# Performance work log

Measured on AMD Instinct MI355X. Metric: run time of the kernel, lower is better.

## Reference

```python
import jax, jax.numpy as jnp
import numpy as np

B, S, DIM = 2, 2048, 1536
H = 12            # n_heads (SIGMA)
HD = DIM // H     # head_dim = 128
SIGMA = 12        # anchors per query: 6 local + 4 strided + 2 global
STRIDE_STEP = 5   # SOPFR


def setup_inputs() -> dict:
    key = jax.random.key(0)
    k0, k1, k2 = jax.random.split(key, 3)
    s = 0.02
    return {
        "x": jax.random.normal(k0, (B, S, DIM), dtype=jnp.float32),
        "Wqkv": jax.random.normal(k1, (DIM, 3 * DIM), dtype=jnp.float32) * s,
        "bqkv": jnp.zeros((3 * DIM,), dtype=jnp.float32),
        "Wout": jax.random.normal(k2, (DIM, DIM), dtype=jnp.float32) * s,
        "bout": jnp.zeros((DIM,), dtype=jnp.float32),
        # Egyptian-fraction init: [W_LOCAL, W_STRIDE, W_GLOBAL] = [1/2, 1/3, 1/6]
        "group_scale": jnp.array([0.5, 1.0 / 3.0, 1.0 / 6.0], dtype=jnp.float32),
    }


def _anchor_indices(seq_len):
    # (S, 12) int32: 6 local offsets, 4 strided offsets, then global {0, S-1}
    pos = jnp.arange(seq_len, dtype=jnp.int32)
    offs = jnp.array([-3, -2, -1, 1, 2, 3,
                      -2 * STRIDE_STEP, -STRIDE_STEP, STRIDE_STEP, 2 * STRIDE_STEP],
                     dtype=jnp.int32)
    a = jnp.clip(pos[:, None] + offs[None, :], 0, seq_len - 1)
    glob = jnp.stack([jnp.zeros_like(pos), jnp.full_like(pos, seq_len - 1)], axis=1)
    return jnp.concatenate([a, glob], axis=1)


def reference(x, Wqkv, bqkv, Wout, bout, group_scale):
    b, s, d_model = x.shape
    # QKV projection -> (3, B, H, S, HD)
    qkv = (x @ Wqkv + bqkv).reshape(b, s, 3, H, HD).transpose(2, 0, 3, 1, 4)
    q, k, v = qkv[0], qkv[1], qkv[2]
    scale = HD ** -0.5

    anchor = _anchor_indices(s)                 # (S, SIGMA)
    k_anchors = jnp.take(k, anchor, axis=2)     # (B, H, S, SIGMA, HD)
    v_anchors = jnp.take(v, anchor, axis=2)     # (B, H, S, SIGMA, HD)

    attn = jnp.einsum('bhsd,bhsad->bhsa', q, k_anchors) * scale

    gw = jax.nn.softmax(group_scale)            # (3,)
    weight_per_anchor = jnp.concatenate([
        jnp.broadcast_to(gw[0], (6,)),   # local
        jnp.broadcast_to(gw[1], (4,)),   # strided
        jnp.broadcast_to(gw[2], (2,)),   # global
    ])                                          # (SIGMA,)
    attn = attn + jnp.log(weight_per_anchor)    # broadcast over (B,H,S,·)

    attn = jax.nn.softmax(attn, axis=-1)
    attn = jnp.nan_to_num(attn, nan=0.0)

    out = jnp.einsum('bhsa,bhsad->bhsd', attn, v_anchors)
    out = out.transpose(0, 2, 1, 3).reshape(b, s, d_model)
    return out @ Wout + bout
```

## Files before the change

kernel.cpp:

```cpp
#include <hip/hip_runtime.h>
#include <hip/hip_bf16.h>
#include <cstdint>
#include <math.h>

#define B_    2
#define S_    2048
#define DIM_  1536
#define H_    12
#define HD_   128
#define TRI_  4608
#define M_    4096

typedef __attribute__((ext_vector_type(8))) __bf16 bf16x8;
typedef __attribute__((ext_vector_type(4))) __bf16 bf16x4;
typedef __attribute__((ext_vector_type(4))) float  floatx4;

typedef __attribute__((address_space(3))) uint8_t       lds_u8;
typedef const __attribute__((address_space(1))) uint8_t glob_u8;

__global__ __launch_bounds__(256) void prep(const float* __restrict__ W1,
                                            __bf16* __restrict__ O1,
                                            const float* __restrict__ W2,
                                            __bf16* __restrict__ O2,
                                            const float* __restrict__ x,
                                            __bf16* __restrict__ x_bf,
                                            float* __restrict__ outz) {
    const int T1 = (TRI_ / 64) * (DIM_ / 64);
    const int T2 = (DIM_ / 64) * (DIM_ / 64);
    const int NC = (M_ * DIM_) / 1024;
    int blk = blockIdx.x;
    const int t = threadIdx.x;

    if (blk >= T1 + T2) {
        blk -= T1 + T2;
        if (blk < NC) {
            int i = blk * 256 + t;
            float4 v = ((const float4*)x)[i];
            bf16x4 o;
            o.x = (__bf16)v.x; o.y = (__bf16)v.y; o.z = (__bf16)v.z; o.w = (__bf16)v.w;
            *(bf16x4*)(x_bf + (size_t)i * 4) = o;
        } else {
            blk -= NC;
            int i = blk * 256 + t;
            ((float4*)outz)[i] = make_float4(0.f, 0.f, 0.f, 0.f);
        }
        return;
    }

    const float* in; __bf16* out; int R, C, c0, r0;
    if (blk < T1) {
        in = W1; out = O1; R = DIM_; C = TRI_;
        c0 = (blk % (TRI_ / 64)) * 64; r0 = (blk / (TRI_ / 64)) * 64;
    } else {
        blk -= T1;
        in = W2; out = O2; R = DIM_; C = DIM_;
        c0 = (blk % (DIM_ / 64)) * 64; r0 = (blk / (DIM_ / 64)) * 64;
    }
    __shared__ float tile[64][65];
    const int c4 = t & 15, r = t >> 4;
    #pragma unroll
    for (int i = 0; i < 64; i += 16) {
        float4 v = *(const float4*)&in[(size_t)(r0 + r + i) * C + c0 + c4 * 4];
        tile[r + i][c4 * 4 + 0] = v.x;
        tile[r + i][c4 * 4 + 1] = v.y;
        tile[r + i][c4 * 4 + 2] = v.z;
        tile[r + i][c4 * 4 + 3] = v.w;
    }
    __syncthreads();
    const int cc = t >> 2, ch = t & 3;
    #pragma unroll
    for (int cho = 0; cho < 8; cho += 4) {
        int chh = ch + cho;
        bf16x8 o;
        #pragma unroll
        for (int k = 0; k < 8; ++k) o[k] = (__bf16)tile[chh * 8 + k][cc];
        *(bf16x8*)&out[(size_t)(c0 + cc) * R + r0 + chh * 8] = o;
    }
}

__global__ __launch_bounds__(256, 3) void gemm_qkv(const __bf16* __restrict__ A,
                                                   const __bf16* __restrict__ Bt,
                                                   const float*  __restrict__ bias,
                                                   __bf16* __restrict__ Cout,
                                                   int Mdim, int Ndim, int Kdim) {
    __shared__ __align__(16) __bf16 sA[128 * 64];
    __shared__ __align__(16) __bf16 sB[192 * 64];

    const int ntiles = Ndim / 192;
    const int tile_n = blockIdx.x % ntiles;
    const int tile_m = blockIdx.x / ntiles;
    const int m0 = tile_m << 7, n0 = tile_n * 192;

    const int tid  = threadIdx.x;
    const int lane = tid & 63;
    const int wave = tid >> 6;
    const int wm = (wave >> 1) * 64;
    const int wn = (wave & 1) * 96;

    floatx4 acc[4][6] = {};

    const int lr8 = lane >> 3;
    const int swz = (((lane & 7) ^ lr8) * 8);
    const int row  = lane & 15;
    const int quad = lane >> 4;
    const int xr   = row & 7;

    for (int k0 = 0; k0 < Kdim; k0 += 64) {
        #pragma unroll
        for (int c = 0; c < 4; ++c) {
            int r0 = wave * 32 + c * 8;
            const __bf16* ga = A + (size_t)(m0 + r0 + lr8) * Kdim + k0 + swz;
            __builtin_amdgcn_global_load_lds((glob_u8*)ga, (lds_u8*)&sA[r0 * 64], 16, 0, 0);
        }
        #pragma unroll
        for (int c = 0; c < 6; ++c) {
            int r0 = wave * 48 + c * 8;
            const __bf16* gb = Bt + (size_t)(n0 + r0 + lr8) * Kdim + k0 + swz;
            __builtin_amdgcn_global_load_lds((glob_u8*)gb, (lds_u8*)&sB[r0 * 64], 16, 0, 0);
        }
        __syncthreads();

        #pragma unroll
        for (int ks = 0; ks < 2; ++ks) {
            const int ko = ((ks * 4 + quad) ^ xr) * 8;
            bf16x8 af[4], bfr[6];
            #pragma unroll
            for (int i = 0; i < 4; ++i)
                af[i] = *(const bf16x8*)&sA[(wm + i * 16 + row) * 64 + ko];
            #pragma unroll
            for (int j = 0; j < 6; ++j)
                bfr[j] = *(const bf16x8*)&sB[(wn + j * 16 + row) * 64 + ko];
            #pragma unroll
            for (int i = 0; i < 4; ++i)
                #pragma unroll
                for (int j = 0; j < 6; ++j)
                    acc[i][j] = __builtin_amdgcn_mfma_f32_16x16x32_bf16(af[i], bfr[j], acc[i][j], 0, 0, 0);
        }
        __syncthreads();
    }

    #pragma unroll
    for (int j = 0; j < 6; ++j) {
        int gc = n0 + wn + j * 16 + row;
        float bv = bias[gc];
        #pragma unroll
        for (int i = 0; i < 4; ++i) {
            #pragma unroll
            for (int r = 0; r < 4; ++r) {
                int gr = m0 + wm + i * 16 + quad * 4 + r;
                Cout[(size_t)gr * Ndim + gc] = (__bf16)(acc[i][j][r] + bv);
            }
        }
    }
}

__global__ __launch_bounds__(256, 3) void gemm_out(const __bf16* __restrict__ A,
                                                   const __bf16* __restrict__ Bt,
                                                   const float*  __restrict__ bias,
                                                   float* __restrict__ Cout,
                                                   int Mdim, int Ndim, int Kdim) {
    __shared__ __align__(16) __bf16 sA[128 * 64];
    __shared__ __align__(16) __bf16 sB[128 * 64];

    const int ntiles = Ndim >> 7;
    const int half = (Mdim >> 7) * ntiles;
    int idx = blockIdx.x;
    const int slice = idx >= half;
    if (slice) idx -= half;
    const int tile_n = idx % ntiles;
    const int tile_m = idx / ntiles;
    const int m0 = tile_m << 7, n0 = tile_n << 7;
    const int kbeg = slice ? (Kdim >> 1) : 0;
    const int kend = kbeg + (Kdim >> 1);

    const int tid  = threadIdx.x;
    const int lane = tid & 63;
    const int wave = tid >> 6;
    const int wm = (wave >> 1) * 64;
    const int wn = (wave & 1) * 64;

    floatx4 acc[4][4] = {};

    const int lr8 = lane >> 3;
    const int swz = (((lane & 7) ^ lr8) * 8);
    const int row  = lane & 15;
    const int quad = lane >> 4;
    const int xr   = row & 7;

    for (int k0 = kbeg; k0 < kend; k0 += 64) {
        #pragma unroll
        for (int c = 0; c < 4; ++c) {
            int r0 = wave * 32 + c * 8;
            const __bf16* ga = A + (size_t)(m0 + r0 + lr8) * Kdim + k0 + swz;
            __builtin_amdgcn_global_load_lds((glob_u8*)ga, (lds_u8*)&sA[r0 * 64], 16, 0, 0);
            const __bf16* gb = Bt + (size_t)(n0 + r0 + lr8) * Kdim + k0 + swz;
            __builtin_amdgcn_global_load_lds((glob_u8*)gb, (lds_u8*)&sB[r0 * 64], 16, 0, 0);
        }
        __syncthreads();

        #pragma unroll
        for (int ks = 0; ks < 2; ++ks) {
            const int ko = ((ks * 4 + quad) ^ xr) * 8;
            bf16x8 af[4], bfr[4];
            #pragma unroll
            for (int i = 0; i < 4; ++i) {
                af[i]  = *(const bf16x8*)&sA[(wm + i * 16 + row) * 64 + ko];
                bfr[i] = *(const bf16x8*)&sB[(wn + i * 16 + row) * 64 + ko];
            }
            #pragma unroll
            for (int i = 0; i < 4; ++i)
                #pragma unroll
                for (int j = 0; j < 4; ++j)
                    acc[i][j] = __builtin_amdgcn_mfma_f32_16x16x32_bf16(af[i], bfr[j], acc[i][j], 0, 0, 0);
        }
        __syncthreads();
    }

    #pragma unroll
    for (int j = 0; j < 4; ++j) {
        int gc = n0 + wn + j * 16 + row;
        float bv = slice ? 0.f : bias[gc];
        #pragma unroll
        for (int i = 0; i < 4; ++i) {
            #pragma unroll
            for (int r = 0; r < 4; ++r) {
                int gr = m0 + wm + i * 16 + quad * 4 + r;
                atomicAdd(&Cout[(size_t)gr * Ndim + gc], acc[i][j][r] + bv);
            }
        }
    }
}

__global__ __launch_bounds__(192) void anchor_attn(const __bf16* __restrict__ qkv,
                                                   const float* __restrict__ group_scale,
                                                   __bf16* __restrict__ attn_out) {
    const int bs = blockIdx.x;
    const int b  = bs >> 11;
    const int s  = bs & 2047;
    const int t  = threadIdx.x;
    const int h  = t >> 4;
    const int tt = t & 15;
    const int d0 = tt * 8;

    float g0 = group_scale[0], g1 = group_scale[1], g2 = group_scale[2];
    float gm = fmaxf(g0, fmaxf(g1, g2));
    float e0 = __expf(g0 - gm), e1 = __expf(g1 - gm), e2 = __expf(g2 - gm);
    float ls = __logf(e0 + e1 + e2);
    float lw0 = g0 - gm - ls, lw1 = g1 - gm - ls, lw2 = g2 - gm - ls;

    const size_t rowbase = (size_t)(b * S_ + s) * TRI_ + h * HD_ + d0;
    bf16x8 qv = *(const bf16x8*)(qkv + rowbase);
    float q[8];
    #pragma unroll
    for (int k = 0; k < 8; ++k) q[k] = (float)qv[k];

    int idxs[12];
    const int offs[10] = {-3, -2, -1, 1, 2, 3, -10, -5, 5, 10};
    #pragma unroll
    for (int a = 0; a < 10; ++a) {
        int tgt = s + offs[a];
        idxs[a] = min(max(tgt, 0), S_ - 1);
    }
    idxs[10] = 0; idxs[11] = S_ - 1;

    const float scale = 0.08838834764831845f;
    float p[12];
    float mx = -1e30f;
    #pragma unroll
    for (int a = 0; a < 12; ++a) {
        const __bf16* kp = qkv + (size_t)(b * S_ + idxs[a]) * TRI_ + DIM_ + h * HD_ + d0;
        bf16x8 kv = *(const bf16x8*)kp;
        float d = 0.f;
        #pragma unroll
        for (int k = 0; k < 8; ++k) d += q[k] * (float)kv[k];
        d += __shfl_xor(d, 1); d += __shfl_xor(d, 2);
        d += __shfl_xor(d, 4); d += __shfl_xor(d, 8);
        float sc = d * scale + (a < 6 ? lw0 : (a < 10 ? lw1 : lw2));
        p[a] = sc;
        mx = fmaxf(mx, sc);
    }
    float l = 0.f;
    #pragma unroll
    for (int a = 0; a < 12; ++a) { p[a] = __expf(p[a] - mx); l += p[a]; }
    float inv = 1.0f / l;

    float o[8] = {};
    #pragma unroll
    for (int a = 0; a < 12; ++a) {
        const __bf16* vp = qkv + (size_t)(b * S_ + idxs[a]) * TRI_ + 2 * DIM_ + h * HD_ + d0;
        bf16x8 vv = *(const bf16x8*)vp;
        #pragma unroll
        for (int k = 0; k < 8; ++k) o[k] += p[a] * (float)vv[k];
    }
    bf16x8 ov;
    #pragma unroll
    for (int k = 0; k < 8; ++k) ov[k] = (__bf16)(o[k] * inv);
    *(bf16x8*)(attn_out + (size_t)(b * S_ + s) * DIM_ + h * HD_ + d0) = ov;
}

extern "C" void kernel_launch(void* const* d_in, const int* in_sizes, int n_in,
                              void* d_out, int out_size, void* d_ws, size_t ws_size,
                              hipStream_t stream) {
    const float* x    = (const float*)d_in[0];
    const float* Wqkv = (const float*)d_in[1];
    const float* bqkv = (const float*)d_in[2];
    const float* Wout = (const float*)d_in[3];
    const float* bout = (const float*)d_in[4];
    const float* gsc  = (const float*)d_in[5];
    float* out = (float*)d_out;

    char* ws = (char*)d_ws;
    __bf16* x_bf   = (__bf16*)(ws);
    __bf16* WqkvT  = (__bf16*)(ws + 12582912);
    __bf16* WoutT  = (__bf16*)(ws + 12582912 + 14155776);
    __bf16* qkv    = (__bf16*)(ws + 12582912 + 14155776 + 4718592);
    __bf16* attn   = (__bf16*)(ws + 12582912 + 14155776 + 4718592 + 37748736);

    {
        int nblk = (TRI_ / 64) * (DIM_ / 64) + (DIM_ / 64) * (DIM_ / 64)
                 + (M_ * DIM_) / 1024 + (M_ * DIM_) / 1024;
        prep<<<nblk, 256, 0, stream>>>(Wqkv, WqkvT, Wout, WoutT, x, x_bf, out);
    }

    gemm_qkv<<<(M_ / 128) * (TRI_ / 192), 256, 0, stream>>>(
        x_bf, WqkvT, bqkv, qkv, M_, TRI_, DIM_);

    anchor_attn<<<B_ * S_, 192, 0, stream>>>(qkv, gsc, attn);

    gemm_out<<<2 * (M_ / 128) * (DIM_ / 128), 256, 0, stream>>>(
        attn, WoutT, bout, out, M_, DIM_, DIM_);
}
```

Baseline: 252.7 us.

## Drop split-K atomics in output GEMM and use 128-wide K tiles

The output projection no longer splits K across two block slices that accumulated with float atomics. Each block now computes its full 128x128 tile over all of K and writes results with plain stores. Because the output no longer needs a zero-initialised buffer, the zeroing pass in the prep kernel is removed. The K tile per stage doubles to 128, with a matching LDS swizzle, so there are half as many barrier-separated iterations. The trade-off is half as many blocks (384 tiles) for the 256-CU part, 64KB of LDS per block, and the dropped occupancy hint of 3 blocks per CU.

New measurement: 230.1 us. 8.9% less time.

```diff
diff --git a/kernel.cpp b/kernel.cpp
--- a/kernel.cpp
+++ b/kernel.cpp
@@ -23,27 +23,19 @@
                                             const float* __restrict__ W2,
                                             __bf16* __restrict__ O2,
                                             const float* __restrict__ x,
-                                            __bf16* __restrict__ x_bf,
-                                            float* __restrict__ outz) {
+                                            __bf16* __restrict__ x_bf) {
     const int T1 = (TRI_ / 64) * (DIM_ / 64);
     const int T2 = (DIM_ / 64) * (DIM_ / 64);
-    const int NC = (M_ * DIM_) / 1024;
     int blk = blockIdx.x;
     const int t = threadIdx.x;
 
     if (blk >= T1 + T2) {
         blk -= T1 + T2;
-        if (blk < NC) {
-            int i = blk * 256 + t;
-            float4 v = ((const float4*)x)[i];
-            bf16x4 o;
-            o.x = (__bf16)v.x; o.y = (__bf16)v.y; o.z = (__bf16)v.z; o.w = (__bf16)v.w;
-            *(bf16x4*)(x_bf + (size_t)i * 4) = o;
-        } else {
-            blk -= NC;
-            int i = blk * 256 + t;
-            ((float4*)outz)[i] = make_float4(0.f, 0.f, 0.f, 0.f);
-        }
+        int i = blk * 256 + t;
+        float4 v = ((const float4*)x)[i];
+        bf16x4 o;
+        o.x = (__bf16)v.x; o.y = (__bf16)v.y; o.z = (__bf16)v.z; o.w = (__bf16)v.w;
+        *(bf16x4*)(x_bf + (size_t)i * 4) = o;
         return;
     }
 
@@ -154,24 +146,18 @@
     }
 }
 
-__global__ __launch_bounds__(256, 3) void gemm_out(const __bf16* __restrict__ A,
-                                                   const __bf16* __restrict__ Bt,
-                                                   const float*  __restrict__ bias,
-                                                   float* __restrict__ Cout,
-                                                   int Mdim, int Ndim, int Kdim) {
-    __shared__ __align__(16) __bf16 sA[128 * 64];
-    __shared__ __align__(16) __bf16 sB[128 * 64];
+__global__ __launch_bounds__(256) void gemm_out(const __bf16* __restrict__ A,
+                                                const __bf16* __restrict__ Bt,
+                                                const float*  __restrict__ bias,
+                                                float* __restrict__ Cout,
+                                                int Mdim, int Ndim, int Kdim) {
+    __shared__ __align__(16) __bf16 sA[128 * 128];
+    __shared__ __align__(16) __bf16 sB[128 * 128];
 
     const int ntiles = Ndim >> 7;
-    const int half = (Mdim >> 7) * ntiles;
-    int idx = blockIdx.x;
-    const int slice = idx >= half;
-    if (slice) idx -= half;
-    const int tile_n = idx % ntiles;
-    const int tile_m = idx / ntiles;
+    const int tile_n = blockIdx.x % ntiles;
+    const int tile_m = blockIdx.x / ntiles;
     const int m0 = tile_m << 7, n0 = tile_n << 7;
-    const int kbeg = slice ? (Kdim >> 1) : 0;
-    const int kend = kbeg + (Kdim >> 1);
 
     const int tid  = threadIdx.x;
     const int lane = tid & 63;
@@ -181,31 +167,34 @@
 
     floatx4 acc[4][4] = {};
 
-    const int lr8 = lane >> 3;
-    const int swz = (((lane & 7) ^ lr8) * 8);
+    const int lr4 = lane >> 4;
+    const int lc  = lane & 15;
+    int swz[4];
+    #pragma unroll
+    for (int v = 0; v < 4; ++v) swz[v] = (lc ^ (v * 4 + lr4)) * 8;
+
     const int row  = lane & 15;
     const int quad = lane >> 4;
-    const int xr   = row & 7;
-
-    for (int k0 = kbeg; k0 < kend; k0 += 64) {
-        #pragma unroll
-        for (int c = 0; c < 4; ++c) {
-            int r0 = wave * 32 + c * 8;
-            const __bf16* ga = A + (size_t)(m0 + r0 + lr8) * Kdim + k0 + swz;
-            __builtin_amdgcn_global_load_lds((glob_u8*)ga, (lds_u8*)&sA[r0 * 64], 16, 0, 0);
-            const __bf16* gb = Bt + (size_t)(n0 + r0 + lr8) * Kdim + k0 + swz;
-            __builtin_amdgcn_global_load_lds((glob_u8*)gb, (lds_u8*)&sB[r0 * 64], 16, 0, 0);
+
+    for (int k0 = 0; k0 < Kdim; k0 += 128) {
+        #pragma unroll
+        for (int c = 0; c < 8; ++c) {
+            int r0 = wave * 32 + c * 4;
+            const __bf16* ga = A + (size_t)(m0 + r0 + lr4) * Kdim + k0 + swz[c & 3];
+            __builtin_amdgcn_global_load_lds((glob_u8*)ga, (lds_u8*)&sA[r0 * 128], 16, 0, 0);
+            const __bf16* gb = Bt + (size_t)(n0 + r0 + lr4) * Kdim + k0 + swz[c & 3];
+            __builtin_amdgcn_global_load_lds((glob_u8*)gb, (lds_u8*)&sB[r0 * 128], 16, 0, 0);
         }
         __syncthreads();
 
         #pragma unroll
-        for (int ks = 0; ks < 2; ++ks) {
-            const int ko = ((ks * 4 + quad) ^ xr) * 8;
+        for (int ks = 0; ks < 4; ++ks) {
+            const int ck = ((ks * 4 + quad) ^ row) * 8;
             bf16x8 af[4], bfr[4];
             #pragma unroll
             for (int i = 0; i < 4; ++i) {
-                af[i]  = *(const bf16x8*)&sA[(wm + i * 16 + row) * 64 + ko];
-                bfr[i] = *(const bf16x8*)&sB[(wn + i * 16 + row) * 64 + ko];
+                af[i]  = *(const bf16x8*)&sA[(wm + i * 16 + row) * 128 + ck];
+                bfr[i] = *(const bf16x8*)&sB[(wn + i * 16 + row) * 128 + ck];
             }
             #pragma unroll
             for (int i = 0; i < 4; ++i)
@@ -219,13 +208,13 @@
     #pragma unroll
     for (int j = 0; j < 4; ++j) {
         int gc = n0 + wn + j * 16 + row;
-        float bv = slice ? 0.f : bias[gc];
+        float bv = bias[gc];
         #pragma unroll
         for (int i = 0; i < 4; ++i) {
             #pragma unroll
             for (int r = 0; r < 4; ++r) {
                 int gr = m0 + wm + i * 16 + quad * 4 + r;
-                atomicAdd(&Cout[(size_t)gr * Ndim + gc], acc[i][j][r] + bv);
+                Cout[(size_t)gr * Ndim + gc] = acc[i][j][r] + bv;
             }
         }
     }
@@ -318,8 +307,8 @@
 
     {
         int nblk = (TRI_ / 64) * (DIM_ / 64) + (DIM_ / 64) * (DIM_ / 64)
-                 + (M_ * DIM_) / 1024 + (M_ * DIM_) / 1024;
-        prep<<<nblk, 256, 0, stream>>>(Wqkv, WqkvT, Wout, WoutT, x, x_bf, out);
+                 + (M_ * DIM_) / 1024;
+        prep<<<nblk, 256, 0, stream>>>(Wqkv, WqkvT, Wout, WoutT, x, x_bf);
     }
 
     gemm_qkv<<<(M_ / 128) * (TRI_ / 192), 256, 0, stream>>>(
@@ -327,6 +316,6 @@
 
     anchor_attn<<<B_ * S_, 192, 0, stream>>>(qkv, gsc, attn);
 
-    gemm_out<<<2 * (M_ / 128) * (DIM_ / 128), 256, 0, stream>>>(
+    gemm_out<<<(M_ / 128) * (DIM_ / 128), 256, 0, stream>>>(
         attn, WoutT, bout, out, M_, DIM_, DIM_);
 }
```
